# Kernel tuning notes

Measured on AMD Instinct MI355X. Metric: run time of the kernel, lower is better.

The kernel has to match this reference:

```python
import jax, jax.numpy as jnp
import numpy as np

DIM = 2560
NUM_HEADS = 40
HEAD_DIM = DIM // NUM_HEADS
SCALE = HEAD_DIM ** -0.5


def setup_inputs() -> dict:
    key = jax.random.key(0)
    k_x, k_wqkv, k_bqkv, k_wp, k_bp = jax.random.split(key, 5)
    B, N = 2, 2048
    x = jax.random.normal(k_x, (B, N, DIM), dtype=jnp.float32)
    s = 1.0 / np.sqrt(DIM)
    w_qkv = jax.random.normal(k_wqkv, (DIM, 3 * DIM), dtype=jnp.float32) * s
    b_qkv = jax.random.normal(k_bqkv, (3 * DIM,), dtype=jnp.float32) * 0.01
    w_proj = jax.random.normal(k_wp, (DIM, DIM), dtype=jnp.float32) * s
    b_proj = jax.random.normal(k_bp, (DIM,), dtype=jnp.float32) * 0.01
    return {"x": x, "w_qkv": w_qkv, "b_qkv": b_qkv, "w_proj": w_proj, "b_proj": b_proj}


def reference(x, w_qkv, b_qkv, w_proj, b_proj):
    B, N, C = x.shape
    qkv = x @ w_qkv + b_qkv                                  # [B,N,3C]
    qkv = qkv.reshape(B, N, 3, NUM_HEADS, HEAD_DIM)
    q = jnp.transpose(qkv[:, :, 0], (0, 2, 1, 3))            # [B,H,N,D]
    k = jnp.transpose(qkv[:, :, 1], (0, 2, 1, 3))
    v = jnp.transpose(qkv[:, :, 2], (0, 2, 1, 3))
    attn = jnp.einsum("bhqd,bhkd->bhqk", q, k) * SCALE       # [B,H,N,N]
    attn = jax.nn.softmax(attn, axis=-1)
    out = jnp.einsum("bhqk,bhkd->bhqd", attn, v)             # [B,H,N,D]
    out = jnp.transpose(out, (0, 2, 1, 3)).reshape(B, N, C)
    return out @ w_proj + b_proj
```

## Files before the change

### kernel.cpp

```cpp
#include <hip/hip_runtime.h>

#define DIMC   2560
#define NHEADS 40
#define HDIM   64
#define BATCH  2
#define SEQ    2048
#define MROWS  (BATCH*SEQ)
#define THREEC (3*DIMC)

typedef short bf16x8 __attribute__((ext_vector_type(8)));
typedef float f32x4  __attribute__((ext_vector_type(4)));

static __device__ __forceinline__ unsigned short f2bf(float f) {
    unsigned int u = __float_as_uint(f);
    u += 0x7FFF + ((u >> 16) & 1);
    return (unsigned short)(u >> 16);
}

__global__ void cast_f32_bf16(const float* __restrict__ src, ushort* __restrict__ dst, int n4) {
    int i = blockIdx.x * blockDim.x + threadIdx.x;
    if (i < n4) {
        float4 v = ((const float4*)src)[i];
        ushort4 o;
        o.x = f2bf(v.x); o.y = f2bf(v.y); o.z = f2bf(v.z); o.w = f2bf(v.w);
        ((ushort4*)dst)[i] = o;
    }
}

template<int MODE>
__global__ __launch_bounds__(256) void gemm_bf16_kernel(
    const ushort* __restrict__ A, const float* __restrict__ Bm,
    const float* __restrict__ bias,
    ushort* __restrict__ q_out, ushort* __restrict__ k_out, ushort* __restrict__ v_out,
    float* __restrict__ c_out, int M, int N, int K)
{
    __shared__ __align__(16) ushort As[128][40];
    __shared__ __align__(16) ushort Bs[128][40];
    const int tid  = threadIdx.x;
    const int lane = tid & 63;
    const int wave = tid >> 6;
    const int wm = (wave >> 1) * 64;
    const int wn = (wave & 1) * 64;
    const int m0 = blockIdx.y * 128;
    const int n0 = blockIdx.x * 128;

    f32x4 acc[4][4] = {};

    for (int k0 = 0; k0 < K; k0 += 32) {
        __syncthreads();
        #pragma unroll
        for (int p = 0; p < 2; ++p) {
            int idx = p * 256 + tid;
            int r = idx >> 2, c = (idx & 3) * 8;
            uint4 v = *(const uint4*)(A + (size_t)(m0 + r) * K + k0 + c);
            *(uint4*)&As[r][c] = v;
        }
        {
            int nb = (tid & 31) * 4;
            int kb = (tid >> 5) * 4;
            const float* bp = Bm + (size_t)(k0 + kb) * N + n0 + nb;
            float4 r0 = *(const float4*)(bp);
            float4 r1 = *(const float4*)(bp + N);
            float4 r2 = *(const float4*)(bp + 2 * (size_t)N);
            float4 r3 = *(const float4*)(bp + 3 * (size_t)N);
            ushort4 c0 = {f2bf(r0.x), f2bf(r1.x), f2bf(r2.x), f2bf(r3.x)};
            ushort4 c1 = {f2bf(r0.y), f2bf(r1.y), f2bf(r2.y), f2bf(r3.y)};
            ushort4 c2 = {f2bf(r0.z), f2bf(r1.z), f2bf(r2.z), f2bf(r3.z)};
            ushort4 c3 = {f2bf(r0.w), f2bf(r1.w), f2bf(r2.w), f2bf(r3.w)};
            *(ushort4*)&Bs[nb + 0][kb] = c0;
            *(ushort4*)&Bs[nb + 1][kb] = c1;
            *(ushort4*)&Bs[nb + 2][kb] = c2;
            *(ushort4*)&Bs[nb + 3][kb] = c3;
        }
        __syncthreads();
        bf16x8 af[4], bfr[4];
        #pragma unroll
        for (int i = 0; i < 4; ++i)
            af[i] = *(const bf16x8*)&As[wm + i * 16 + (lane & 15)][(lane >> 4) * 8];
        #pragma unroll
        for (int j = 0; j < 4; ++j)
            bfr[j] = *(const bf16x8*)&Bs[wn + j * 16 + (lane & 15)][(lane >> 4) * 8];
        #pragma unroll
        for (int i = 0; i < 4; ++i)
            #pragma unroll
            for (int j = 0; j < 4; ++j)
                acc[i][j] = __builtin_amdgcn_mfma_f32_16x16x32_bf16(af[i], bfr[j], acc[i][j], 0, 0, 0);
    }

    const int rbase = m0 + wm + ((lane >> 4) << 2);
    const int cbase = n0 + wn + (lane & 15);
    #pragma unroll
    for (int i = 0; i < 4; ++i) {
        #pragma unroll
        for (int j = 0; j < 4; ++j) {
            int ccol = cbase + j * 16;
            float bv = bias[ccol];
            #pragma unroll
            for (int r = 0; r < 4; ++r) {
                int row = rbase + i * 16 + r;
                float val = acc[i][j][r] + bv;
                if (MODE == 0) {
                    int which = ccol / DIMC;
                    int cc = ccol - which * DIMC;
                    int h = cc >> 6, d = cc & 63;
                    int b = row >> 11, n = row & 2047;
                    if (which == 0) {
                        size_t idx = (((size_t)(b * NHEADS + h)) * SEQ + n) * HDIM + d;
                        q_out[idx] = f2bf(val * 0.18033688011112042f);
                    } else if (which == 1) {
                        size_t idx = (((size_t)(b * NHEADS + h)) * SEQ + n) * HDIM + d;
                        k_out[idx] = f2bf(val);
                    } else {
                        size_t idx = (((size_t)(b * NHEADS + h)) * HDIM + d) * SEQ + n;
                        v_out[idx] = f2bf(val);
                    }
                } else {
                    c_out[(size_t)row * N + ccol] = val;
                }
            }
        }
    }
}

__global__ __launch_bounds__(256) void attn_kernel(
    const ushort* __restrict__ Q, const ushort* __restrict__ K,
    const ushort* __restrict__ VT, ushort* __restrict__ Oattn)
{
    __shared__ __align__(16) ushort Ps[128][88];
    const int tid  = threadIdx.x;
    const int lane = tid & 63;
    const int quad = lane >> 4;
    const int l15  = lane & 15;
    const int wave = tid >> 6;
    const int bh = blockIdx.y;
    const int b = bh / NHEADS, h = bh % NHEADS;
    const int q0 = blockIdx.x * 128;
    const int wq = wave * 32;
    const size_t base = (size_t)bh * SEQ * HDIM;
    const size_t tbase = base;

    bf16x8 qf[2][2];
    #pragma unroll
    for (int i = 0; i < 2; ++i)
        #pragma unroll
        for (int kk = 0; kk < 2; ++kk)
            qf[i][kk] = *(const bf16x8*)(Q + base + (size_t)(q0 + wq + i * 16 + l15) * HDIM
                                         + kk * 32 + quad * 8);

    float mstate[2] = {-INFINITY, -INFINITY};
    float lstate[2] = {0.f, 0.f};
    f32x4 o[4][2] = {};

    for (int t = 0; t < SEQ / 64; ++t) {
        const int k0 = t * 64;
        f32x4 s[2][4] = {};
        #pragma unroll
        for (int j = 0; j < 4; ++j) {
            #pragma unroll
            for (int kk = 0; kk < 2; ++kk) {
                bf16x8 kf = *(const bf16x8*)(K + base + (size_t)(k0 + j * 16 + l15) * HDIM
                                             + kk * 32 + quad * 8);
                #pragma unroll
                for (int i = 0; i < 2; ++i)
                    s[i][j] = __builtin_amdgcn_mfma_f32_16x16x32_bf16(kf, qf[i][kk], s[i][j], 0, 0, 0);
            }
        }
        bf16x8 vf[4][2];
        #pragma unroll
        for (int dj = 0; dj < 4; ++dj)
            #pragma unroll
            for (int kk = 0; kk < 2; ++kk)
                vf[dj][kk] = *(const bf16x8*)(VT + tbase + (size_t)(dj * 16 + l15) * SEQ
                                              + k0 + kk * 32 + quad * 8);
        float alpha[2];
        #pragma unroll
        for (int i = 0; i < 2; ++i) {
            float cm = s[i][0][0];
            #pragma unroll
            for (int j = 0; j < 4; ++j)
                #pragma unroll
                for (int r = 0; r < 4; ++r)
                    cm = fmaxf(cm, s[i][j][r]);
            cm = fmaxf(cm, __shfl_xor(cm, 16, 64));
            cm = fmaxf(cm, __shfl_xor(cm, 32, 64));
            float mnew = fmaxf(mstate[i], cm);
            alpha[i] = __builtin_amdgcn_exp2f(mstate[i] - mnew);
            mstate[i] = mnew;
            float rs = 0.f;
            #pragma unroll
            for (int j = 0; j < 4; ++j)
                #pragma unroll
                for (int r = 0; r < 4; ++r) {
                    float p = __builtin_amdgcn_exp2f(s[i][j][r] - mnew);
                    s[i][j][r] = p;
                    rs += p;
                }
            rs += __shfl_xor(rs, 16, 64);
            rs += __shfl_xor(rs, 32, 64);
            lstate[i] = lstate[i] * alpha[i] + rs;
            #pragma unroll
            for (int dj = 0; dj < 4; ++dj)
                #pragma unroll
                for (int r = 0; r < 4; ++r)
                    o[dj][i][r] *= alpha[i];
        }
        #pragma unroll
        for (int i = 0; i < 2; ++i)
            #pragma unroll
            for (int j = 0; j < 4; ++j) {
                ushort4 pk = {f2bf(s[i][j][0]), f2bf(s[i][j][1]), f2bf(s[i][j][2]), f2bf(s[i][j][3])};
                *(ushort4*)&Ps[wq + i * 16 + l15][j * 16 + quad * 4] = pk;
            }
        #pragma unroll
        for (int kk = 0; kk < 2; ++kk) {
            bf16x8 pf[2];
            #pragma unroll
            for (int i = 0; i < 2; ++i)
                pf[i] = *(const bf16x8*)&Ps[wq + i * 16 + l15][kk * 32 + quad * 8];
            #pragma unroll
            for (int dj = 0; dj < 4; ++dj)
                #pragma unroll
                for (int i = 0; i < 2; ++i)
                    o[dj][i] = __builtin_amdgcn_mfma_f32_16x16x32_bf16(vf[dj][kk], pf[i], o[dj][i], 0, 0, 0);
        }
    }
    #pragma unroll
    for (int i = 0; i < 2; ++i) {
        float inv = 1.f / lstate[i];
        int qrow = q0 + wq + i * 16 + l15;
        size_t orow = ((size_t)b * SEQ + qrow) * DIMC + (size_t)h * HDIM;
        #pragma unroll
        for (int dj = 0; dj < 4; ++dj) {
            ushort4 ok = {f2bf(o[dj][i][0] * inv), f2bf(o[dj][i][1] * inv),
                          f2bf(o[dj][i][2] * inv), f2bf(o[dj][i][3] * inv)};
            *(ushort4*)(Oattn + orow + dj * 16 + quad * 4) = ok;
        }
    }
}

extern "C" void kernel_launch(void* const* d_in, const int* in_sizes, int n_in,
                              void* d_out, int out_size, void* d_ws, size_t ws_size,
                              hipStream_t stream) {
    const float* x      = (const float*)d_in[0];
    const float* w_qkv  = (const float*)d_in[1];
    const float* b_qkv  = (const float*)d_in[2];
    const float* w_proj = (const float*)d_in[3];
    const float* b_proj = (const float*)d_in[4];
    float* out = (float*)d_out;

    char* ws = (char*)d_ws;
    const size_t sz_x   = (size_t)MROWS * DIMC * 2;
    const size_t sz_qkv = (size_t)BATCH * NHEADS * SEQ * HDIM * 2;
    ushort* xb    = (ushort*)ws;                 ws += sz_x;
    ushort* Qb    = (ushort*)ws;                 ws += sz_qkv;
    ushort* Kb    = (ushort*)ws;                 ws += sz_qkv;
    ushort* Vtb   = (ushort*)ws;                 ws += sz_qkv;
    ushort* attnb = (ushort*)ws;                 ws += sz_x;

    int n4 = MROWS * DIMC / 4;
    cast_f32_bf16<<<n4 / 256, 256, 0, stream>>>(x, xb, n4);

    gemm_bf16_kernel<0><<<dim3(THREEC / 128, MROWS / 128), 256, 0, stream>>>(
        xb, w_qkv, b_qkv, Qb, Kb, Vtb, nullptr, MROWS, THREEC, DIMC);

    attn_kernel<<<dim3(SEQ / 128, BATCH * NHEADS), 256, 0, stream>>>(Qb, Kb, Vtb, attnb);

    gemm_bf16_kernel<1><<<dim3(DIMC / 128, MROWS / 128), 256, 0, stream>>>(
        attnb, w_proj, b_proj, nullptr, nullptr, nullptr, out, MROWS, DIMC, DIMC);
}
```

Before: 953.9 us.

## Pre-transpose weights to bf16 and load GEMM tiles directly into LDS

Adds a transpose-and-cast kernel that turns each fp32 weight matrix into a bf16 N-major copy once per call. The GEMM then loads both operands straight into LDS with global_load_lds, instead of converting fp32 weights per tile in registers and storing them through VGPRs. The workspace is reused: the attention output overwrites xb and the transposed projection weights overwrite Qb. The LDS tile loses its padding, which risks bank conflicts on the fragment reads, and the extra transpose passes add weight traffic.

```diff
diff --git a/kernel.cpp b/kernel.cpp
--- a/kernel.cpp
+++ b/kernel.cpp
@@ -17,6 +17,12 @@
     return (unsigned short)(u >> 16);
 }
 
+static __device__ __forceinline__ void gload_lds16(const ushort* g, ushort* l) {
+    __builtin_amdgcn_global_load_lds(
+        (const __attribute__((address_space(1))) void*)g,
+        (__attribute__((address_space(3))) void*)l, 16, 0, 0);
+}
+
 __global__ void cast_f32_bf16(const float* __restrict__ src, ushort* __restrict__ dst, int n4) {
     int i = blockIdx.x * blockDim.x + threadIdx.x;
     if (i < n4) {
@@ -27,59 +33,71 @@
     }
 }
 
+__global__ __launch_bounds__(256) void transpose_cast(
+    const float* __restrict__ W, ushort* __restrict__ WT, int K, int N)
+{
+    __shared__ float Ls[64][65];
+    const int t = threadIdx.x;
+    const int n0 = blockIdx.x * 64, k0 = blockIdx.y * 64;
+    #pragma unroll
+    for (int p = 0; p < 4; ++p) {
+        int idx = p * 256 + t;
+        int r = idx >> 4, c4 = (idx & 15) * 4;
+        float4 v = *(const float4*)(W + (size_t)(k0 + r) * N + n0 + c4);
+        Ls[r][c4] = v.x; Ls[r][c4 + 1] = v.y; Ls[r][c4 + 2] = v.z; Ls[r][c4 + 3] = v.w;
+    }
+    __syncthreads();
+    #pragma unroll
+    for (int p = 0; p < 4; ++p) {
+        int idx = p * 256 + t;
+        int n = idx >> 4, kc = (idx & 15) * 4;
+        ushort4 o = {f2bf(Ls[kc][n]), f2bf(Ls[kc + 1][n]), f2bf(Ls[kc + 2][n]), f2bf(Ls[kc + 3][n])};
+        *(ushort4*)(WT + (size_t)(n0 + n) * K + k0 + kc) = o;
+    }
+}
+
 template<int MODE>
-__global__ __launch_bounds__(256) void gemm_bf16_kernel(
-    const ushort* __restrict__ A, const float* __restrict__ Bm,
+__global__ __launch_bounds__(256) void gemm_bt(
+    const ushort* __restrict__ A, const ushort* __restrict__ BT,
     const float* __restrict__ bias,
     ushort* __restrict__ q_out, ushort* __restrict__ k_out, ushort* __restrict__ v_out,
     float* __restrict__ c_out, int M, int N, int K)
 {
-    __shared__ __align__(16) ushort As[128][40];
-    __shared__ __align__(16) ushort Bs[128][40];
+    __shared__ __align__(16) ushort As[128 * 32];
+    __shared__ __align__(16) ushort Bs[128 * 32];
     const int tid  = threadIdx.x;
     const int lane = tid & 63;
     const int wave = tid >> 6;
+    const int l15  = lane & 15, quad = lane >> 4;
     const int wm = (wave >> 1) * 64;
     const int wn = (wave & 1) * 64;
     const int m0 = blockIdx.y * 128;
     const int n0 = blockIdx.x * 128;
 
+    const int srow = wave * 32 + (lane >> 2);
+    const int scol = (lane & 3) * 8;
+    const ushort* ga = A  + (size_t)(m0 + srow) * K + scol;
+    const ushort* gb = BT + (size_t)(n0 + srow) * K + scol;
+    ushort* la = &As[(wave * 32) * 32];
+    ushort* lb = &Bs[(wave * 32) * 32];
+
     f32x4 acc[4][4] = {};
 
     for (int k0 = 0; k0 < K; k0 += 32) {
         __syncthreads();
         #pragma unroll
         for (int p = 0; p < 2; ++p) {
-            int idx = p * 256 + tid;
-            int r = idx >> 2, c = (idx & 3) * 8;
-            uint4 v = *(const uint4*)(A + (size_t)(m0 + r) * K + k0 + c);
-            *(uint4*)&As[r][c] = v;
-        }
-        {
-            int nb = (tid & 31) * 4;
-            int kb = (tid >> 5) * 4;
-            const float* bp = Bm + (size_t)(k0 + kb) * N + n0 + nb;
-            float4 r0 = *(const float4*)(bp);
-            float4 r1 = *(const float4*)(bp + N);
-            float4 r2 = *(const float4*)(bp + 2 * (size_t)N);
-            float4 r3 = *(const float4*)(bp + 3 * (size_t)N);
-            ushort4 c0 = {f2bf(r0.x), f2bf(r1.x), f2bf(r2.x), f2bf(r3.x)};
-            ushort4 c1 = {f2bf(r0.y), f2bf(r1.y), f2bf(r2.y), f2bf(r3.y)};
-            ushort4 c2 = {f2bf(r0.z), f2bf(r1.z), f2bf(r2.z), f2bf(r3.z)};
-            ushort4 c3 = {f2bf(r0.w), f2bf(r1.w), f2bf(r2.w), f2bf(r3.w)};
-            *(ushort4*)&Bs[nb + 0][kb] = c0;
-            *(ushort4*)&Bs[nb + 1][kb] = c1;
-            *(ushort4*)&Bs[nb + 2][kb] = c2;
-            *(ushort4*)&Bs[nb + 3][kb] = c3;
+            gload_lds16(ga + k0 + (size_t)(p * 16) * K, la + p * 16 * 32);
+            gload_lds16(gb + k0 + (size_t)(p * 16) * K, lb + p * 16 * 32);
         }
         __syncthreads();
         bf16x8 af[4], bfr[4];
         #pragma unroll
         for (int i = 0; i < 4; ++i)
-            af[i] = *(const bf16x8*)&As[wm + i * 16 + (lane & 15)][(lane >> 4) * 8];
+            af[i] = *(const bf16x8*)&As[(wm + i * 16 + l15) * 32 + quad * 8];
         #pragma unroll
         for (int j = 0; j < 4; ++j)
-            bfr[j] = *(const bf16x8*)&Bs[wn + j * 16 + (lane & 15)][(lane >> 4) * 8];
+            bfr[j] = *(const bf16x8*)&Bs[(wn + j * 16 + l15) * 32 + quad * 8];
         #pragma unroll
         for (int i = 0; i < 4; ++i)
             #pragma unroll
@@ -87,8 +105,8 @@
                 acc[i][j] = __builtin_amdgcn_mfma_f32_16x16x32_bf16(af[i], bfr[j], acc[i][j], 0, 0, 0);
     }
 
-    const int rbase = m0 + wm + ((lane >> 4) << 2);
-    const int cbase = n0 + wn + (lane & 15);
+    const int rbase = m0 + wm + (quad << 2);
+    const int cbase = n0 + wn + l15;
     #pragma unroll
     for (int i = 0; i < 4; ++i) {
         #pragma unroll
@@ -137,7 +155,6 @@
     const int q0 = blockIdx.x * 128;
     const int wq = wave * 32;
     const size_t base = (size_t)bh * SEQ * HDIM;
-    const size_t tbase = base;
 
     bf16x8 qf[2][2];
     #pragma unroll
@@ -170,7 +187,7 @@
         for (int dj = 0; dj < 4; ++dj)
             #pragma unroll
             for (int kk = 0; kk < 2; ++kk)
-                vf[dj][kk] = *(const bf16x8*)(VT + tbase + (size_t)(dj * 16 + l15) * SEQ
+                vf[dj][kk] = *(const bf16x8*)(VT + base + (size_t)(dj * 16 + l15) * SEQ
                                               + k0 + kk * 32 + quad * 8);
         float alpha[2];
         #pragma unroll
@@ -248,23 +265,29 @@
     const float* b_proj = (const float*)d_in[4];
     float* out = (float*)d_out;
 
-    char* ws = (char*)d_ws;
+    char* p = (char*)d_ws;
     const size_t sz_x   = (size_t)MROWS * DIMC * 2;
     const size_t sz_qkv = (size_t)BATCH * NHEADS * SEQ * HDIM * 2;
-    ushort* xb    = (ushort*)ws;                 ws += sz_x;
-    ushort* Qb    = (ushort*)ws;                 ws += sz_qkv;
-    ushort* Kb    = (ushort*)ws;                 ws += sz_qkv;
-    ushort* Vtb   = (ushort*)ws;                 ws += sz_qkv;
-    ushort* attnb = (ushort*)ws;                 ws += sz_x;
+    ushort* xb    = (ushort*)p;  p += sz_x;
+    ushort* Qb    = (ushort*)p;  p += sz_qkv;
+    ushort* Kb    = (ushort*)p;  p += sz_qkv;
+    ushort* Vtb   = (ushort*)p;  p += sz_qkv;
+    ushort* wqkvT = (ushort*)p;  p += (size_t)THREEC * DIMC * 2;
+    ushort* attnb  = xb;
+    ushort* wprojT = Qb;
 
     int n4 = MROWS * DIMC / 4;
     cast_f32_bf16<<<n4 / 256, 256, 0, stream>>>(x, xb, n4);
 
-    gemm_bf16_kernel<0><<<dim3(THREEC / 128, MROWS / 128), 256, 0, stream>>>(
-        xb, w_qkv, b_qkv, Qb, Kb, Vtb, nullptr, MROWS, THREEC, DIMC);
+    transpose_cast<<<dim3(THREEC / 64, DIMC / 64), 256, 0, stream>>>(w_qkv, wqkvT, DIMC, THREEC);
+
+    gemm_bt<0><<<dim3(THREEC / 128, MROWS / 128), 256, 0, stream>>>(
+        xb, wqkvT, b_qkv, Qb, Kb, Vtb, nullptr, MROWS, THREEC, DIMC);
 
     attn_kernel<<<dim3(SEQ / 128, BATCH * NHEADS), 256, 0, stream>>>(Qb, Kb, Vtb, attnb);
 
-    gemm_bf16_kernel<1><<<dim3(DIMC / 128, MROWS / 128), 256, 0, stream>>>(
-        attnb, w_proj, b_proj, nullptr, nullptr, nullptr, out, MROWS, DIMC, DIMC);
-}
+    transpose_cast<<<dim3(DIMC / 64, DIMC / 64), 256, 0, stream>>>(w_proj, wprojT, DIMC, DIMC);
+
+    gemm_bt<1><<<dim3(DIMC / 128, MROWS / 128), 256, 0, stream>>>(
+        attnb, wprojT, b_proj, nullptr, nullptr, nullptr, out, MROWS, DIMC, DIMC);
+}
```

Result: faster. 819.1 us (-14.1%).
